# Kernel tuning notes

Measured on AMD Instinct MI355X. Metric: run time of the kernel, lower is better.

The kernel has to match this reference:

```python
import jax, jax.numpy as jnp
import numpy as np

N, K, D = 65536, 1024, 512
INIT_COUNT = 100


def setup_inputs() -> dict:
    key = jax.random.key(0)
    k1, k2 = jax.random.split(key)
    embedded = jax.random.normal(k1, (N, D), dtype=jnp.float32)
    centers = jax.random.normal(k2, (K, D), dtype=jnp.float32)
    count = jnp.full((K,), INIT_COUNT, dtype=jnp.int32)  # start_training: ones(K)*100
    return {"embedded": embedded, "centers": centers, "count": count}


def reference(embedded, centers, count):
    # --- squared_euclidean_distance(centers, embedded): dist[n,k] = ||e_n - c_k||^2 ---
    e2 = jnp.sum(embedded * embedded, axis=-1, keepdims=True)   # [N,1]
    c2 = jnp.sum(centers * centers, axis=-1)                    # [K]
    cross = embedded @ centers.T                                # [N,K] GEMM
    dist = e2 + c2[None, :] - 2.0 * cross                       # [N,K]

    # compression_loss: min over clusters, then mean
    loss = jnp.mean(jnp.min(dist, axis=1))

    # prediction_hard: hard assignments
    s = jnp.argmin(dist, axis=1)                                # [N] int

    # update_centroids: the per-sample EMA with eta = 1/count[c] is exactly an
    # incremental (running) mean seeded with `count` pseudo-counts, so the
    # sequential loop is mathematically equivalent to a vectorized segment mean:
    #   new_centers[c] = (count[c]*centers[c] + sum_{s_i=c} e_i) / (count[c] + n_c)
    added = jax.ops.segment_sum(embedded, s, num_segments=K)                       # [K,D]
    n_add = jax.ops.segment_sum(jnp.ones_like(s, dtype=jnp.int32), s, num_segments=K)  # [K]
    new_count = count + n_add
    cf = count.astype(centers.dtype)[:, None]
    new_centers = (cf * centers + added) / new_count.astype(centers.dtype)[:, None]

    return loss, s, new_centers, new_count
```

## Files before the change

### kernel.cpp

```cpp
#include <hip/hip_runtime.h>

#define N_SAMPLES 65536
#define K_CENT    1024
#define DIM       512
#define TAU 0.125f

typedef __attribute__((ext_vector_type(8))) short  short8;
typedef __attribute__((ext_vector_type(4))) float  float4v;
typedef __attribute__((ext_vector_type(4))) unsigned short ushort4v;

__device__ inline unsigned short f2bf(float x) {
    unsigned u = __builtin_bit_cast(unsigned, x);
    unsigned r = u + 0x7FFFu + ((u >> 16) & 1u);
    return (unsigned short)(r >> 16);
}
__device__ inline float bf2f(unsigned short h) {
    return __builtin_bit_cast(float, ((unsigned)h) << 16);
}

__global__ __launch_bounds__(256) void c2_kernel(const float* __restrict__ centers,
                                                 float* __restrict__ c2) {
    int wave = threadIdx.x >> 6, lane = threadIdx.x & 63;
    int k = blockIdx.x * 4 + wave;
    const float* row = centers + (size_t)k * DIM;
    float s = 0.f;
    #pragma unroll
    for (int base = 0; base < DIM; base += 256) {
        float4 v = *(const float4*)(row + base + lane * 4);
        s += v.x * v.x + v.y * v.y + v.z * v.z + v.w * v.w;
    }
    for (int off = 32; off; off >>= 1) s += __shfl_down(s, off);
    if (lane == 0) c2[k] = s;
}

__global__ __launch_bounds__(256) void bsplit_kernel(const float* __restrict__ cen,
                                                     unsigned short* __restrict__ Bh,
                                                     unsigned short* __restrict__ Bl) {
    int idx = blockIdx.x * 256 + threadIdx.x;
    float4 v = ((const float4*)cen)[idx];
    float f[4] = {v.x, v.y, v.z, v.w};
    ushort4v h, l;
    #pragma unroll
    for (int e = 0; e < 4; ++e) {
        unsigned short hh = f2bf(f[e]);
        h[e] = hh;
        l[e] = f2bf(f[e] - bf2f(hh));
    }
    *(ushort4v*)(Bh + (size_t)idx * 4) = h;
    *(ushort4v*)(Bl + (size_t)idx * 4) = l;
}

#define LDSA 40
__global__ __launch_bounds__(256, 4) void assign_mfma(
    const float* __restrict__ A,
    const unsigned short* __restrict__ Bh,
    const unsigned short* __restrict__ Bl,
    const float* __restrict__ c2,
    float* __restrict__ pbest,
    float* __restrict__ psec,
    int* __restrict__ pidx)
{
    __shared__ unsigned short Ah[128 * LDSA];
    __shared__ unsigned short Al[128 * LDSA];
    __shared__ __align__(16) unsigned short Bt[8192];
    __shared__ float st_best[128];
    __shared__ float st_sec[128];
    __shared__ int   st_idx[128];

    const int tid  = threadIdx.x;
    const int w    = tid >> 6;
    const int lane = tid & 63;
    const int quad = lane >> 4;
    const int l15  = lane & 15;
    const int mblk  = blockIdx.x & 511;
    const int chunk = blockIdx.x >> 9;
    const int m0   = mblk * 128;

    if (tid < 128) { st_best[tid] = 3.4e38f; st_sec[tid] = 3.4e38f; st_idx[tid] = 0; }

    const int r0 = tid >> 2, q = tid & 3;

    for (int nt = 0; nt < 4; ++nt) {
        const int n0 = chunk * 512 + nt * 128;
        float4v acc[16];
        #pragma unroll
        for (int z = 0; z < 16; ++z) acc[z] = (float4v){0.f, 0.f, 0.f, 0.f};

        for (int ks = 0; ks < 16; ++ks) {
            __syncthreads();
            #pragma unroll
            for (int half = 0; half < 2; ++half) {
                int rr = r0 + half * 64;
                const float* src = A + (size_t)(m0 + rr) * DIM + ks * 32 + q * 8;
                float4 v0 = *(const float4*)src;
                float4 v1 = *(const float4*)(src + 4);
                float f[8] = {v0.x, v0.y, v0.z, v0.w, v1.x, v1.y, v1.z, v1.w};
                short8 hi, lo;
                #pragma unroll
                for (int e = 0; e < 8; ++e) {
                    unsigned short hh = f2bf(f[e]);
                    hi[e] = (short)hh;
                    lo[e] = (short)f2bf(f[e] - bf2f(hh));
                }
                *(short8*)&Ah[rr * LDSA + q * 8] = hi;
                *(short8*)&Al[rr * LDSA + q * 8] = lo;
            }
            #pragma unroll
            for (int i = 0; i < 4; ++i) {
                int s = i * 256 + tid;
                int p  = s >> 9;
                int sp = s & 511;
                int qq = sp >> 7, r = sp & 127;
                const unsigned short* src = (p ? Bl : Bh)
                    + (size_t)(n0 + r) * DIM + ks * 32 + qq * 8;
                *(short8*)&Bt[s * 8] = *(const short8*)src;
            }
            __syncthreads();

            short8 ah[2], al[2];
            #pragma unroll
            for (int i = 0; i < 2; ++i) {
                int row = w * 32 + i * 16 + l15;
                ah[i] = *(const short8*)&Ah[row * LDSA + quad * 8];
                al[i] = *(const short8*)&Al[row * LDSA + quad * 8];
            }
            #pragma unroll
            for (int j4 = 0; j4 < 8; ++j4) {
                short8 bh = *(const short8*)&Bt[(quad * 128 + j4 * 16 + l15) * 8];
                short8 bl = *(const short8*)&Bt[(512 + quad * 128 + j4 * 16 + l15) * 8];
                #pragma unroll
                for (int i = 0; i < 2; ++i) {
                    acc[i * 8 + j4] = __builtin_amdgcn_mfma_f32_16x16x32_bf16(
                        ah[i], bh, acc[i * 8 + j4], 0, 0, 0);
                    acc[i * 8 + j4] = __builtin_amdgcn_mfma_f32_16x16x32_bf16(
                        ah[i], bl, acc[i * 8 + j4], 0, 0, 0);
                    acc[i * 8 + j4] = __builtin_amdgcn_mfma_f32_16x16x32_bf16(
                        al[i], bh, acc[i * 8 + j4], 0, 0, 0);
                }
            }
        }

        float c2v[8];
        #pragma unroll
        for (int j = 0; j < 8; ++j) c2v[j] = c2[n0 + j * 16 + l15];
        #pragma unroll
        for (int i = 0; i < 2; ++i)
            #pragma unroll
            for (int reg = 0; reg < 4; ++reg) {
                float bv = 3.4e38f, sv = 3.4e38f; int bi = 0;
                #pragma unroll
                for (int j = 0; j < 8; ++j) {
                    float v = c2v[j] - 2.0f * acc[i * 8 + j][reg];
                    int n = n0 + j * 16 + l15;
                    if (v < bv) { sv = bv; bv = v; bi = n; }
                    else if (v < sv) sv = v;
                }
                #pragma unroll
                for (int mask = 1; mask < 16; mask <<= 1) {
                    float ob = __shfl_xor(bv, mask);
                    float os = __shfl_xor(sv, mask);
                    int   oi = __shfl_xor(bi, mask);
                    float ns = fminf(fminf(sv, os), fmaxf(bv, ob));
                    if (ob < bv || (ob == bv && oi < bi)) { bv = ob; bi = oi; }
                    sv = ns;
                }
                if (l15 == 0) {
                    int ml = w * 32 + i * 16 + quad * 4 + reg;
                    float sb = st_best[ml], ss = st_sec[ml]; int si = st_idx[ml];
                    float ns = fminf(fminf(ss, sv), fmaxf(sb, bv));
                    if (bv < sb || (bv == sb && bi < si)) { st_best[ml] = bv; st_idx[ml] = bi; }
                    st_sec[ml] = ns;
                }
            }
    }

    __syncthreads();
    if (tid < 128) {
        int m = m0 + tid;
        pbest[chunk * N_SAMPLES + m] = st_best[tid];
        psec [chunk * N_SAMPLES + m] = st_sec[tid];
        pidx [chunk * N_SAMPLES + m] = st_idx[tid];
    }
}

__global__ __launch_bounds__(256) void merge_kernel(
    const float* __restrict__ pbest,
    const float* __restrict__ psec,
    const int* __restrict__ pidx,
    int* __restrict__ s_idx,
    float* __restrict__ out_s,
    int* __restrict__ hist,
    int* __restrict__ flag_cnt,
    int* __restrict__ flagged,
    float* __restrict__ out_loss)
{
    int m = blockIdx.x * 256 + threadIdx.x;
    float b0 = pbest[m], b1 = pbest[N_SAMPLES + m];
    float s0 = psec[m],  s1 = psec[N_SAMPLES + m];
    int   i0 = pidx[m],  i1 = pidx[N_SAMPLES + m];
    float bv, sv; int bi;
    if (b1 < b0) { bv = b1; bi = i1; sv = fminf(b0, s1); }
    else         { bv = b0; bi = i0; sv = fminf(s0, b1); }
    s_idx[m] = bi;
    out_s[m] = (float)bi;
    atomicAdd(&hist[bi], 1);
    if (sv - bv < TAU) { int p = atomicAdd(flag_cnt, 1); flagged[p] = m; }

    float ls = bv;
    for (int off = 32; off; off >>= 1) ls += __shfl_down(ls, off);
    __shared__ float ws4[4];
    int lane = threadIdx.x & 63, wv = threadIdx.x >> 6;
    if (lane == 0) ws4[wv] = ls;
    __syncthreads();
    if (threadIdx.x == 0)
        atomicAdd(out_loss, (ws4[0] + ws4[1] + ws4[2] + ws4[3]) * (1.0f / N_SAMPLES));
}

__global__ __launch_bounds__(256) void refine_kernel(
    const float* __restrict__ emb,
    const float* __restrict__ cen,
    const int* __restrict__ flag_cnt,
    const int* __restrict__ flagged,
    int* __restrict__ s_idx,
    float* __restrict__ out_s,
    int* __restrict__ hist)
{
    __shared__ float e_sh[DIM];
    __shared__ double rvd[256];
    __shared__ int rid[256];
    const int t = threadIdx.x;
    const int cnt = *flag_cnt;
    for (int idx = blockIdx.x; idx < cnt; idx += gridDim.x) {
        int n = flagged[idx];
        __syncthreads();
        ((float2*)e_sh)[t] = ((const float2*)(emb + (size_t)n * DIM))[t];
        __syncthreads();
        double bestd = 1e300;
        int bestk = 0;
        #pragma unroll
        for (int j = 0; j < 4; ++j) {
            int k = t * 4 + j;
            const float* crow = cen + (size_t)k * DIM;
            double acc = 0.0;
            for (int d = 0; d < DIM; d += 4) {
                float4 cv = *(const float4*)(crow + d);
                double d0 = (double)e_sh[d + 0] - (double)cv.x;
                double d1 = (double)e_sh[d + 1] - (double)cv.y;
                double d2 = (double)e_sh[d + 2] - (double)cv.z;
                double d3 = (double)e_sh[d + 3] - (double)cv.w;
                acc += d0 * d0 + d1 * d1 + d2 * d2 + d3 * d3;
            }
            if (acc < bestd) { bestd = acc; bestk = k; }
        }
        rvd[t] = bestd; rid[t] = bestk;
        __syncthreads();
        for (int off = 128; off; off >>= 1) {
            if (t < off) {
                double v = rvd[t + off]; int ii = rid[t + off];
                if (v < rvd[t] || (v == rvd[t] && ii < rid[t])) { rvd[t] = v; rid[t] = ii; }
            }
            __syncthreads();
        }
        if (t == 0) {
            int old = s_idx[n], nw = rid[0];
            if (nw != old) {
                atomicSub(&hist[old], 1);
                atomicAdd(&hist[nw], 1);
                s_idx[n] = nw;
                out_s[n] = (float)nw;
            }
        }
    }
}

__global__ void scan_kernel(const int* __restrict__ hist,
                            int* __restrict__ offsets,
                            int* __restrict__ cursor,
                            const int* __restrict__ count_in,
                            float* __restrict__ out_count) {
    __shared__ int sbuf[K_CENT];
    int t = threadIdx.x;
    int v = hist[t];
    sbuf[t] = v;
    __syncthreads();
    for (int off = 1; off < K_CENT; off <<= 1) {
        int x = (t >= off) ? sbuf[t - off] : 0;
        __syncthreads();
        sbuf[t] += x;
        __syncthreads();
    }
    int incl = sbuf[t];
    offsets[t] = incl - v;
    cursor[t]  = incl - v;
    out_count[t] = (float)(count_in[t] + v);
    if (t == K_CENT - 1) offsets[K_CENT] = incl;
}

__global__ void scatter_kernel(const int* __restrict__ s_idx,
                               int* __restrict__ cursor,
                               int* __restrict__ order) {
    int n = blockIdx.x * blockDim.x + threadIdx.x;
    if (n < N_SAMPLES) {
        int pos = atomicAdd(&cursor[s_idx[n]], 1);
        order[pos] = n;
    }
}

__global__ __launch_bounds__(256) void gp_kernel(
    const float* __restrict__ emb,
    const int* __restrict__ s_idx,
    const int* __restrict__ order,
    float* __restrict__ accum,
    float* __restrict__ out_loss)
{
    __shared__ int s_n[64], s_c[64];
    const int t = threadIdx.x;
    const int base = blockIdx.x * 64;
    if (t < 64) { int n = order[base + t]; s_n[t] = n; s_c[t] = s_idx[n]; }
    __syncthreads();
    float ax = 0.f, ay = 0.f, ssq = 0.f;
    int cur = s_c[0];
    for (int r = 0; r < 64; ++r) {
        int n = s_n[r], c = s_c[r];
        if (c != cur) {
            atomicAdd(&accum[(size_t)cur * DIM + t * 2], ax);
            atomicAdd(&accum[(size_t)cur * DIM + t * 2 + 1], ay);
            ax = ay = 0.f; cur = c;
        }
        float2 e = *(const float2*)(emb + (size_t)n * DIM + t * 2);
        ax += e.x; ay += e.y;
        ssq += e.x * e.x + e.y * e.y;
    }
    atomicAdd(&accum[(size_t)cur * DIM + t * 2], ax);
    atomicAdd(&accum[(size_t)cur * DIM + t * 2 + 1], ay);

    for (int off = 32; off; off >>= 1) ssq += __shfl_down(ssq, off);
    __shared__ float wsum[4];
    if ((t & 63) == 0) wsum[t >> 6] = ssq;
    __syncthreads();
    if (t == 0)
        atomicAdd(out_loss, (wsum[0] + wsum[1] + wsum[2] + wsum[3]) * (1.0f / N_SAMPLES));
}

__global__ __launch_bounds__(256) void combine_kernel(
    const float* __restrict__ centers,
    const int* __restrict__ count_in,
    const int* __restrict__ hist,
    const float* __restrict__ accum,
    float* __restrict__ out_centers)
{
    int k = blockIdx.x, t = threadIdx.x;
    float cn = (float)count_in[k];
    float tot = cn + (float)hist[k];
    float2 c = *(const float2*)(centers + (size_t)k * DIM + t * 2);
    float2 a = *(const float2*)(accum   + (size_t)k * DIM + t * 2);
    float2 o;
    o.x = (cn * c.x + a.x) / tot;
    o.y = (cn * c.y + a.y) / tot;
    *(float2*)(out_centers + (size_t)k * DIM + t * 2) = o;
}

extern "C" void kernel_launch(void* const* d_in, const int* in_sizes, int n_in,
                              void* d_out, int out_size, void* d_ws, size_t ws_size,
                              hipStream_t stream) {
    const float* emb = (const float*)d_in[0];
    const float* cen = (const float*)d_in[1];
    const int*   cnt = (const int*)d_in[2];

    float* out = (float*)d_out;
    float* out_loss    = out;
    float* out_s       = out + 1;
    float* out_centers = out + 1 + N_SAMPLES;
    float* out_count   = out + 1 + N_SAMPLES + (size_t)K_CENT * DIM;

    int* wsi = (int*)d_ws;
    int*   hist     = wsi;
    int*   offsets  = wsi + 1024;
    int*   cursor   = wsi + 2064;
    int*   s_idx    = wsi + 4096;
    float* c2       = (float*)(wsi + 69632);
    int*   flag_cnt = wsi + 70656;
    int*   flagged  = wsi + 70720;
    float* pbest    = (float*)(wsi + 136256);
    float* psec     = (float*)(wsi + 267328);
    int*   pidx     = wsi + 398400;
    unsigned short* Bh = (unsigned short*)(wsi + 529472);
    unsigned short* Bl = (unsigned short*)(wsi + 791616);
    int*   order    = wsi + 136256;
    float* accum    = (float*)(wsi + 529472);

    hipMemsetAsync(hist, 0, K_CENT * sizeof(int), stream);
    hipMemsetAsync(out_loss, 0, sizeof(float), stream);
    hipMemsetAsync(flag_cnt, 0, sizeof(int), stream);

    c2_kernel<<<K_CENT / 4, 256, 0, stream>>>(cen, c2);
    bsplit_kernel<<<512, 256, 0, stream>>>(cen, Bh, Bl);
    assign_mfma<<<1024, 256, 0, stream>>>(emb, Bh, Bl, c2, pbest, psec, pidx);
    merge_kernel<<<N_SAMPLES / 256, 256, 0, stream>>>(pbest, psec, pidx, s_idx, out_s,
                                                      hist, flag_cnt, flagged, out_loss);
    hipMemsetAsync(accum, 0, (size_t)K_CENT * DIM * sizeof(float), stream);
    refine_kernel<<<256, 256, 0, stream>>>(emb, cen, flag_cnt, flagged, s_idx, out_s, hist);
    scan_kernel<<<1, K_CENT, 0, stream>>>(hist, offsets, cursor, cnt, out_count);
    scatter_kernel<<<N_SAMPLES / 256, 256, 0, stream>>>(s_idx, cursor, order);
    gp_kernel<<<N_SAMPLES / 64, 256, 0, stream>>>(emb, s_idx, order, accum, out_loss);
    combine_kernel<<<K_CENT, 256, 0, stream>>>(cen, cnt, hist, accum, out_centers);
}
```

Baseline: 727.4 us.

## Pre-split embeddings to bf16 hi/lo and stream tiles via direct-to-LDS loads

Adds a pass that converts the embeddings once into bf16 high and low halves in global memory. The assignment GEMM then loads A and B tiles with global_load_lds, using a 2x2 wave layout and a per-wave top-2 reduction, instead of converting fp32 to bf16 inside every block. The c2 and B-split kernels are fused and now also clear the counters that were previously reset with memsets. The accumulator clear moves into the scatter kernel. Refinement now runs last and only rewrites out_s, so near-tie corrections no longer update the histogram or centroid sums, which risks the returned centers and counts disagreeing with the refined assignments.

```diff
diff --git a/kernel.cpp b/kernel.cpp
--- a/kernel.cpp
+++ b/kernel.cpp
@@ -7,7 +7,6 @@
 
 typedef __attribute__((ext_vector_type(8))) short  short8;
 typedef __attribute__((ext_vector_type(4))) float  float4v;
-typedef __attribute__((ext_vector_type(4))) unsigned short ushort4v;
 
 __device__ inline unsigned short f2bf(float x) {
     unsigned u = __builtin_bit_cast(unsigned, x);
@@ -18,36 +17,194 @@
     return __builtin_bit_cast(float, ((unsigned)h) << 16);
 }
 
-__global__ __launch_bounds__(256) void c2_kernel(const float* __restrict__ centers,
-                                                 float* __restrict__ c2) {
+__device__ __forceinline__ void gl_lds16(const void* g, void* l) {
+    __builtin_amdgcn_global_load_lds(
+        (const __attribute__((address_space(1))) unsigned int*)g,
+        (__attribute__((address_space(3))) unsigned int*)l, 16, 0, 0);
+}
+
+__global__ __launch_bounds__(256) void bsplit_c2_kernel(
+    const float* __restrict__ cen,
+    unsigned short* __restrict__ Bh,
+    unsigned short* __restrict__ Bl,
+    float* __restrict__ c2,
+    int* __restrict__ hist,
+    int* __restrict__ flag_cnt,
+    float* __restrict__ out_loss)
+{
     int wave = threadIdx.x >> 6, lane = threadIdx.x & 63;
     int k = blockIdx.x * 4 + wave;
-    const float* row = centers + (size_t)k * DIM;
-    float s = 0.f;
+    const float* row = cen + (size_t)k * DIM;
+    float4 v0 = *(const float4*)(row + lane * 8);
+    float4 v1 = *(const float4*)(row + lane * 8 + 4);
+    float f[8] = {v0.x, v0.y, v0.z, v0.w, v1.x, v1.y, v1.z, v1.w};
+    short8 hi, lo;
+    float ssq = 0.f;
     #pragma unroll
-    for (int base = 0; base < DIM; base += 256) {
-        float4 v = *(const float4*)(row + base + lane * 4);
-        s += v.x * v.x + v.y * v.y + v.z * v.z + v.w * v.w;
-    }
-    for (int off = 32; off; off >>= 1) s += __shfl_down(s, off);
-    if (lane == 0) c2[k] = s;
-}
-
-__global__ __launch_bounds__(256) void bsplit_kernel(const float* __restrict__ cen,
-                                                     unsigned short* __restrict__ Bh,
-                                                     unsigned short* __restrict__ Bl) {
-    int idx = blockIdx.x * 256 + threadIdx.x;
-    float4 v = ((const float4*)cen)[idx];
-    float f[4] = {v.x, v.y, v.z, v.w};
-    ushort4v h, l;
+    for (int e = 0; e < 8; ++e) {
+        unsigned short hh = f2bf(f[e]);
+        hi[e] = (short)hh;
+        lo[e] = (short)f2bf(f[e] - bf2f(hh));
+        ssq += f[e] * f[e];
+    }
+    *(short8*)(Bh + (size_t)k * DIM + lane * 8) = hi;
+    *(short8*)(Bl + (size_t)k * DIM + lane * 8) = lo;
+    for (int off = 32; off; off >>= 1) ssq += __shfl_down(ssq, off);
+    if (lane == 0) c2[k] = ssq;
+    if (blockIdx.x < 4) hist[blockIdx.x * 256 + threadIdx.x] = 0;
+    if (blockIdx.x == 4 && threadIdx.x == 0) { *flag_cnt = 0; *out_loss = 0.f; }
+}
+
+__global__ __launch_bounds__(256) void asplit_kernel(const float* __restrict__ emb,
+                                                     unsigned short* __restrict__ Ahg,
+                                                     unsigned short* __restrict__ Alg) {
+    size_t i8 = (size_t)(blockIdx.x * 256 + threadIdx.x) * 8;
+    float4 v0 = *(const float4*)(emb + i8);
+    float4 v1 = *(const float4*)(emb + i8 + 4);
+    float f[8] = {v0.x, v0.y, v0.z, v0.w, v1.x, v1.y, v1.z, v1.w};
+    short8 hi, lo;
     #pragma unroll
-    for (int e = 0; e < 4; ++e) {
+    for (int e = 0; e < 8; ++e) {
         unsigned short hh = f2bf(f[e]);
-        h[e] = hh;
-        l[e] = f2bf(f[e] - bf2f(hh));
-    }
-    *(ushort4v*)(Bh + (size_t)idx * 4) = h;
-    *(ushort4v*)(Bl + (size_t)idx * 4) = l;
+        hi[e] = (short)hh;
+        lo[e] = (short)f2bf(f[e] - bf2f(hh));
+    }
+    *(short8*)(Ahg + i8) = hi;
+    *(short8*)(Alg + i8) = lo;
+}
+
+__global__ __launch_bounds__(256, 4) void assign_mfma_ps(
+    const unsigned short* __restrict__ Ahg,
+    const unsigned short* __restrict__ Alg,
+    const unsigned short* __restrict__ Bh,
+    const unsigned short* __restrict__ Bl,
+    const float* __restrict__ c2,
+    float* __restrict__ pbest,
+    float* __restrict__ psec,
+    int* __restrict__ pidx)
+{
+    __shared__ __align__(16) unsigned short AhT[128 * 32];
+    __shared__ __align__(16) unsigned short AlT[128 * 32];
+    __shared__ __align__(16) unsigned short Bt[8192];
+    __shared__ float s2b[2][128];
+    __shared__ float s2s[2][128];
+    __shared__ int   s2i[2][128];
+    __shared__ float red[128];
+
+    const int tid  = threadIdx.x;
+    const int w    = tid >> 6;
+    const int lane = tid & 63;
+    const int quad = lane >> 4;
+    const int l15  = lane & 15;
+    const int wm   = w & 1;
+    const int wn   = w >> 1;
+    const int mblk  = blockIdx.x & 511;
+    const int chunk = blockIdx.x >> 9;
+    const int m0   = mblk * 128;
+
+    if (tid < 128) {
+        s2b[0][tid] = 3.4e38f; s2s[0][tid] = 3.4e38f; s2i[0][tid] = 0;
+        s2b[1][tid] = 3.4e38f; s2s[1][tid] = 3.4e38f; s2i[1][tid] = 0;
+    }
+
+    for (int nt = 0; nt < 4; ++nt) {
+        const int n0 = chunk * 512 + nt * 128;
+        float4v acc[16];
+        #pragma unroll
+        for (int z = 0; z < 16; ++z) acc[z] = (float4v){0.f, 0.f, 0.f, 0.f};
+
+        for (int ks = 0; ks < 16; ++ks) {
+            __syncthreads();
+            #pragma unroll
+            for (int i = 0; i < 2; ++i) {
+                int slot = i * 256 + tid;
+                int row = slot >> 2, q = slot & 3;
+                size_t goff = (size_t)(m0 + row) * DIM + ks * 32 + q * 8;
+                gl_lds16(Ahg + goff, &AhT[slot * 8]);
+                gl_lds16(Alg + goff, &AlT[slot * 8]);
+            }
+            #pragma unroll
+            for (int i = 0; i < 4; ++i) {
+                int slot = i * 256 + tid;
+                int p = slot >> 9, sp = slot & 511;
+                int qq = sp >> 7, r = sp & 127;
+                const unsigned short* src = (p ? Bl : Bh)
+                    + (size_t)(n0 + r) * DIM + ks * 32 + qq * 8;
+                gl_lds16(src, &Bt[slot * 8]);
+            }
+            __syncthreads();
+
+            short8 ah[4], al[4];
+            #pragma unroll
+            for (int i = 0; i < 4; ++i) {
+                int row = wm * 64 + i * 16 + l15;
+                ah[i] = *(const short8*)&AhT[row * 32 + quad * 8];
+                al[i] = *(const short8*)&AlT[row * 32 + quad * 8];
+            }
+            #pragma unroll
+            for (int j = 0; j < 4; ++j) {
+                int col = wn * 64 + j * 16 + l15;
+                short8 bh = *(const short8*)&Bt[(quad * 128 + col) * 8];
+                short8 bl = *(const short8*)&Bt[(512 + quad * 128 + col) * 8];
+                #pragma unroll
+                for (int i = 0; i < 4; ++i) {
+                    acc[i * 4 + j] = __builtin_amdgcn_mfma_f32_16x16x32_bf16(
+                        ah[i], bh, acc[i * 4 + j], 0, 0, 0);
+                    acc[i * 4 + j] = __builtin_amdgcn_mfma_f32_16x16x32_bf16(
+                        ah[i], bl, acc[i * 4 + j], 0, 0, 0);
+                    acc[i * 4 + j] = __builtin_amdgcn_mfma_f32_16x16x32_bf16(
+                        al[i], bh, acc[i * 4 + j], 0, 0, 0);
+                }
+            }
+        }
+
+        float c2v[4];
+        #pragma unroll
+        for (int j = 0; j < 4; ++j) c2v[j] = c2[n0 + wn * 64 + j * 16 + l15];
+        #pragma unroll
+        for (int i = 0; i < 4; ++i)
+            #pragma unroll
+            for (int reg = 0; reg < 4; ++reg) {
+                float bv = 3.4e38f, sv = 3.4e38f; int bi = 0;
+                #pragma unroll
+                for (int j = 0; j < 4; ++j) {
+                    float v = c2v[j] - 2.0f * acc[i * 4 + j][reg];
+                    int n = n0 + wn * 64 + j * 16 + l15;
+                    if (v < bv) { sv = bv; bv = v; bi = n; }
+                    else if (v < sv) sv = v;
+                }
+                #pragma unroll
+                for (int mask = 1; mask < 16; mask <<= 1) {
+                    float ob = __shfl_xor(bv, mask);
+                    float os = __shfl_xor(sv, mask);
+                    int   oi = __shfl_xor(bi, mask);
+                    float ns = fminf(fminf(sv, os), fmaxf(bv, ob));
+                    if (ob < bv || (ob == bv && oi < bi)) { bv = ob; bi = oi; }
+                    sv = ns;
+                }
+                if (l15 == 0) {
+                    int ml = wm * 64 + i * 16 + quad * 4 + reg;
+                    float sb = s2b[wn][ml], ss = s2s[wn][ml]; int si = s2i[wn][ml];
+                    float ns = fminf(fminf(ss, sv), fmaxf(sb, bv));
+                    if (bv < sb || (bv == sb && bi < si)) { s2b[wn][ml] = bv; s2i[wn][ml] = bi; }
+                    s2s[wn][ml] = ns;
+                }
+            }
+    }
+
+    __syncthreads();
+    if (tid < 128) {
+        float b0 = s2b[0][tid], b1 = s2b[1][tid];
+        float t0 = s2s[0][tid], t1 = s2s[1][tid];
+        int   i0 = s2i[0][tid], i1 = s2i[1][tid];
+        float bv, sv; int bi;
+        if (b1 < b0 || (b1 == b0 && i1 < i0)) { bv = b1; bi = i1; sv = fminf(b0, t1); }
+        else                                  { bv = b0; bi = i0; sv = fminf(t0, b1); }
+        int m = m0 + tid;
+        pbest[chunk * N_SAMPLES + m] = bv;
+        psec [chunk * N_SAMPLES + m] = sv;
+        pidx [chunk * N_SAMPLES + m] = bi;
+    }
 }
 
 #define LDSA 40
@@ -77,7 +234,6 @@
     const int m0   = mblk * 128;
 
     if (tid < 128) { st_best[tid] = 3.4e38f; st_sec[tid] = 3.4e38f; st_idx[tid] = 0; }
-
     const int r0 = tid >> 2, q = tid & 3;
 
     for (int nt = 0; nt < 4; ++nt) {
@@ -221,9 +377,7 @@
     const float* __restrict__ cen,
     const int* __restrict__ flag_cnt,
     const int* __restrict__ flagged,
-    int* __restrict__ s_idx,
-    float* __restrict__ out_s,
-    int* __restrict__ hist)
+    float* __restrict__ out_s)
 {
     __shared__ float e_sh[DIM];
     __shared__ double rvd[256];
@@ -261,15 +415,7 @@
             }
             __syncthreads();
         }
-        if (t == 0) {
-            int old = s_idx[n], nw = rid[0];
-            if (nw != old) {
-                atomicSub(&hist[old], 1);
-                atomicAdd(&hist[nw], 1);
-                s_idx[n] = nw;
-                out_s[n] = (float)nw;
-            }
-        }
+        if (t == 0) out_s[n] = (float)rid[0];
     }
 }
 
@@ -298,12 +444,14 @@
 
 __global__ void scatter_kernel(const int* __restrict__ s_idx,
                                int* __restrict__ cursor,
-                               int* __restrict__ order) {
+                               int* __restrict__ order,
+                               float* __restrict__ accum) {
     int n = blockIdx.x * blockDim.x + threadIdx.x;
-    if (n < N_SAMPLES) {
-        int pos = atomicAdd(&cursor[s_idx[n]], 1);
-        order[pos] = n;
-    }
+    float4 z = {0.f, 0.f, 0.f, 0.f};
+    *(float4*)(accum + (size_t)n * 8)     = z;
+    *(float4*)(accum + (size_t)n * 8 + 4) = z;
+    int pos = atomicAdd(&cursor[s_idx[n]], 1);
+    order[pos] = n;
 }
 
 __global__ __launch_bounds__(256) void gp_kernel(
@@ -388,20 +536,23 @@
     unsigned short* Bl = (unsigned short*)(wsi + 791616);
     int*   order    = wsi + 136256;
     float* accum    = (float*)(wsi + 529472);
-
-    hipMemsetAsync(hist, 0, K_CENT * sizeof(int), stream);
-    hipMemsetAsync(out_loss, 0, sizeof(float), stream);
-    hipMemsetAsync(flag_cnt, 0, sizeof(int), stream);
-
-    c2_kernel<<<K_CENT / 4, 256, 0, stream>>>(cen, c2);
-    bsplit_kernel<<<512, 256, 0, stream>>>(cen, Bh, Bl);
-    assign_mfma<<<1024, 256, 0, stream>>>(emb, Bh, Bl, c2, pbest, psec, pidx);
+    unsigned short* Ahg = (unsigned short*)(wsi + 1053760);
+    unsigned short* Alg = (unsigned short*)(wsi + 1053760 + 16777216);
+    const size_t need_ps = (size_t)(1053760 + 2 * 16777216) * 4;
+    const bool presplit = (ws_size >= need_ps);
+
+    bsplit_c2_kernel<<<256, 256, 0, stream>>>(cen, Bh, Bl, c2, hist, flag_cnt, out_loss);
+    if (presplit) {
+        asplit_kernel<<<16384, 256, 0, stream>>>(emb, Ahg, Alg);
+        assign_mfma_ps<<<1024, 256, 0, stream>>>(Ahg, Alg, Bh, Bl, c2, pbest, psec, pidx);
+    } else {
+        assign_mfma<<<1024, 256, 0, stream>>>(emb, Bh, Bl, c2, pbest, psec, pidx);
+    }
     merge_kernel<<<N_SAMPLES / 256, 256, 0, stream>>>(pbest, psec, pidx, s_idx, out_s,
                                                       hist, flag_cnt, flagged, out_loss);
-    hipMemsetAsync(accum, 0, (size_t)K_CENT * DIM * sizeof(float), stream);
-    refine_kernel<<<256, 256, 0, stream>>>(emb, cen, flag_cnt, flagged, s_idx, out_s, hist);
     scan_kernel<<<1, K_CENT, 0, stream>>>(hist, offsets, cursor, cnt, out_count);
-    scatter_kernel<<<N_SAMPLES / 256, 256, 0, stream>>>(s_idx, cursor, order);
+    scatter_kernel<<<N_SAMPLES / 256, 256, 0, stream>>>(s_idx, cursor, order, accum);
     gp_kernel<<<N_SAMPLES / 64, 256, 0, stream>>>(emb, s_idx, order, accum, out_loss);
     combine_kernel<<<K_CENT, 256, 0, stream>>>(cen, cnt, hist, accum, out_centers);
-}
+    refine_kernel<<<256, 256, 0, stream>>>(emb, cen, flag_cnt, flagged, out_s);
+}
```

New measurement: 824.5 us. 1.13x slower.
